# Optimization experiments

Measured on AMD Instinct MI355X. Metric: run time of the kernel, lower is better.

## Reference

```python
import jax, jax.numpy as jnp
import numpy as np

B = 16384   # batch
S = 6       # fixed number of ABR frequencies
H = 8       # num_heads
HD = 64     # head_dim
D = H * HD  # model width = head_dim * num_heads


def _pe(d):
    # FrequencyPositionalEncoding: pe[i, 0::2] = sin(f_i * div), pe[i, 1::2] = cos(f_i * div)
    freqs = np.array([6.0, 12.0, 18.0, 24.0, 30.0, 0.0], np.float32) / 30.0
    div = np.exp(np.arange(0, d, 2, dtype=np.float32) * (-np.log(10000.0) / d))
    pe = np.zeros((S, d), np.float32)
    pe[:, 0::2] = np.sin(freqs[:, None] * div)
    pe[:, 1::2] = np.cos(freqs[:, None] * div)
    return jnp.asarray(pe)


def _freq_bias():
    # adjacent-frequency bias 0.1, octave pairs (0,1),(1,3) overwritten to 0.05
    b = np.zeros((S, S), np.float32)
    for i in range(S - 1):
        b[i, i + 1] = 0.1
        b[i + 1, i] = 0.1
    for i, j in [(0, 1), (1, 3)]:
        b[i, j] = 0.05
        b[j, i] = 0.05
    return jnp.asarray(b)


def setup_inputs() -> dict:
    key = jax.random.key(0)
    ks = jax.random.split(key, 6)

    def w(k, shape, s=0.05):
        return jax.random.normal(k, shape, jnp.float32) * s

    return {
        "x": jax.random.normal(ks[0], (B, S), jnp.float32),
        "W_in": w(ks[1], (1, D)), "b_in": jnp.zeros((D,), jnp.float32),
        "Wq": w(ks[2], (D, D)), "bq": jnp.zeros((D,), jnp.float32),
        "Wk": w(ks[3], (D, D)), "bk": jnp.zeros((D,), jnp.float32),
        "Wv": w(ks[4], (D, D)), "bv": jnp.zeros((D,), jnp.float32),
        "Wo": w(ks[5], (D, 1)), "bo": jnp.zeros((1,), jnp.float32),
        "gamma": jnp.ones((D,), jnp.float32),
        "beta": jnp.zeros((D,), jnp.float32),
    }


def reference(x, W_in, b_in, Wq, bq, Wk, bk, Wv, bv, Wo, bo, gamma, beta):
    Bn, Sn = x.shape
    Dn = gamma.shape[0]
    hd = Dn // H
    # input projection: scalar token -> D   (Linear(1, D))
    tok = x[..., None] * W_in[0] + b_in                      # (B, S, D)
    tok = tok + _pe(Dn)[None]                                # frequency positional encoding
    # LayerNorm (eps=1e-5)
    mu = tok.mean(-1, keepdims=True)
    var = tok.var(-1, keepdims=True)
    tok = (tok - mu) * jax.lax.rsqrt(var + 1e-5) * gamma + beta
    # q/k/v projections, split heads
    q = (tok @ Wq + bq).reshape(Bn, Sn, H, hd)
    k = (tok @ Wk + bk).reshape(Bn, Sn, H, hd)
    v = (tok @ Wv + bv).reshape(Bn, Sn, H, hd)
    scores = jnp.einsum('bihd,bjhd->bhij', q, k) * (hd ** -0.5)
    scores = scores + _freq_bias()[None, None]               # (B, H, S, S)
    attn = jax.nn.softmax(scores, axis=-1)                   # dropout = identity (eval)
    attended = jnp.einsum('bhij,bjhd->bihd', attn, v).reshape(Bn, Sn, Dn)
    out = (attended @ Wo + bo)[..., 0] + x                   # (B, S) residual
    return out, attn.mean(axis=1)
```

## Files before the change

### kernel.cpp

```cpp
#include <hip/hip_runtime.h>
#include <math.h>

#define WS_STATS 0
#define WS_T     16
#define WS_LS    600

__constant__ float FREQ_BIAS[36] = {
    0.0f, 0.05f, 0.0f, 0.0f, 0.0f, 0.0f,
    0.05f, 0.0f, 0.1f, 0.05f, 0.0f, 0.0f,
    0.0f, 0.1f, 0.0f, 0.1f, 0.0f, 0.0f,
    0.0f, 0.05f, 0.1f, 0.0f, 0.1f, 0.0f,
    0.0f, 0.0f, 0.0f, 0.1f, 0.0f, 0.1f,
    0.0f, 0.0f, 0.0f, 0.0f, 0.1f, 0.0f
};

__global__ __launch_bounds__(512) void kP(const float* __restrict__ W_in,
                                          const float* __restrict__ b_in,
                                          const float* __restrict__ gamma,
                                          const float* __restrict__ beta,
                                          float* __restrict__ ws)
{
    __shared__ float red[13][8];
    const int d = threadIdx.x, wave = d >> 6, lane = d & 63;

    const float k_ln = 0.0179889457300305367f;
    const float freqs[6] = {0.2f, 0.4f, 0.6f, 0.8f, 1.0f, 0.0f};
    const float wd = W_in[d];
    const float gm = gamma[d];
    const float bt = beta[d];
    const float bi = b_in[d];
    const float dv = __expf(-(float)(d & ~1) * k_ln);
    const bool odd = (d & 1);
    float c[6];
    #pragma unroll
    for (int s = 0; s < 6; ++s) {
        float ph = freqs[s] * dv;
        c[s] = bi + (odd ? __cosf(ph) : __sinf(ph));
    }

    float sums[7];
    sums[0] = wd;
    #pragma unroll
    for (int s = 0; s < 6; ++s) sums[1 + s] = c[s];
    #pragma unroll
    for (int m = 1; m < 64; m <<= 1) {
        #pragma unroll
        for (int k = 0; k < 7; ++k) sums[k] += __shfl_xor(sums[k], m, 64);
    }
    if (lane == 0) {
        #pragma unroll
        for (int k = 0; k < 7; ++k) red[k][wave] = sums[k];
    }
    __syncthreads();
    float mw = 0.f, mc[6] = {0.f, 0.f, 0.f, 0.f, 0.f, 0.f};
    #pragma unroll
    for (int j = 0; j < 8; ++j) mw += red[0][j];
    mw *= (1.0f / 512.0f);
    #pragma unroll
    for (int s = 0; s < 6; ++s) {
        float t = 0.f;
        #pragma unroll
        for (int j = 0; j < 8; ++j) t += red[1 + s][j];
        mc[s] = t * (1.0f / 512.0f);
    }
    __syncthreads();

    const float hw = wd - mw;
    float hc[6];
    #pragma unroll
    for (int s = 0; s < 6; ++s) hc[s] = c[s] - mc[s];

    float moms[13];
    moms[0] = hw * hw;
    #pragma unroll
    for (int s = 0; s < 6; ++s) { moms[1 + s] = hw * hc[s]; moms[7 + s] = hc[s] * hc[s]; }
    #pragma unroll
    for (int m = 1; m < 64; m <<= 1) {
        #pragma unroll
        for (int k = 0; k < 13; ++k) moms[k] += __shfl_xor(moms[k], m, 64);
    }
    if (lane == 0) {
        #pragma unroll
        for (int k = 0; k < 13; ++k) red[k][wave] = moms[k];
    }
    __syncthreads();
    if (d < 13) {
        float t = 0.f;
        #pragma unroll
        for (int j = 0; j < 8; ++j) t += red[d][j];
        ws[WS_STATS + d] = t * (1.0f / 512.0f);
    }

    float4 f0 = make_float4(hw * gm, hc[0] * gm, hc[1] * gm, hc[2] * gm);
    float4 f1 = make_float4(hc[3] * gm, hc[4] * gm, hc[5] * gm, bt);
    *(float4*)&ws[WS_LS + d * 8]     = f0;
    *(float4*)&ws[WS_LS + d * 8 + 4] = f1;
}

__global__ __launch_bounds__(512) void kA(
    const float* __restrict__ Wq, const float* __restrict__ bq,
    const float* __restrict__ Wk, const float* __restrict__ bk,
    const float* __restrict__ Wv, const float* __restrict__ bv,
    const float* __restrict__ ws, float* __restrict__ part)
{
    __shared__ float ls_s[64 * 8];
    __shared__ float partial[8][8][64];

    const int tid = threadIdx.x, wave = tid >> 6, lane = tid & 63;
    const int bid = blockIdx.x;
    const int rc = bid & 7, cg = (bid >> 3) & 7, p = bid >> 6;

    ls_s[tid] = ws[WS_LS + rc * 512 + tid];
    __syncthreads();

    const float* W  = (p == 0) ? Wq : ((p == 1) ? Wk : Wv);
    const float* bb = (p == 0) ? bq : ((p == 1) ? bk : bv);
    const int col = (cg << 6) | lane;
    const int lr0 = wave << 3;
    const int row0 = (rc << 6) | lr0;

    float acc[8] = {0.f, 0.f, 0.f, 0.f, 0.f, 0.f, 0.f, 0.f};
    #pragma unroll
    for (int rr = 0; rr < 8; ++rr) {
        const float wv = W[(row0 + rr) * 512 + col];
        const float4 f0 = *(const float4*)&ls_s[(lr0 + rr) * 8];
        const float4 f1 = *(const float4*)&ls_s[(lr0 + rr) * 8 + 4];
        acc[0] = fmaf(wv, f0.x, acc[0]);
        acc[1] = fmaf(wv, f0.y, acc[1]);
        acc[2] = fmaf(wv, f0.z, acc[2]);
        acc[3] = fmaf(wv, f0.w, acc[3]);
        acc[4] = fmaf(wv, f1.x, acc[4]);
        acc[5] = fmaf(wv, f1.y, acc[5]);
        acc[6] = fmaf(wv, f1.z, acc[6]);
        acc[7] = fmaf(wv, f1.w, acc[7]);
    }
    #pragma unroll
    for (int v = 0; v < 8; ++v) partial[wave][v][lane] = acc[v];
    __syncthreads();

    {
        const int v = tid >> 6, cx = tid & 63;
        float t = 0.f;
        #pragma unroll
        for (int w = 0; w < 8; ++w) t += partial[w][v][cx];
        if (v == 7 && rc == 0) t += bb[(cg << 6) | cx];
        part[(size_t)bid * 512 + tid] = t;
    }
}

__global__ __launch_bounds__(256) void kB(const float* __restrict__ part,
                                          const float* __restrict__ Wo,
                                          float* __restrict__ ws)
{
    __shared__ float ab[24][65];
    const int tid = threadIdx.x;
    const int h = blockIdx.x;

    for (int e = tid; e < 24 * 64; e += 256) {
        const int vp = e >> 6, c = e & 63;
        const int p = vp >> 3, v = vp & 7;
        const int stripe = p * 8 + h;
        float t = 0.f;
        #pragma unroll
        for (int rcx = 0; rcx < 8; ++rcx)
            t += part[(size_t)(stripe * 8 + rcx) * 512 + v * 64 + c];
        ab[vp][c] = t;
    }
    __syncthreads();

    if (tid < 64) {
        const int a = tid >> 3, b2 = tid & 7;
        float acc = 0.f;
        #pragma unroll
        for (int c = 0; c < 64; ++c)
            acc = fmaf(ab[a][c], ab[8 + b2][c], acc);
        ws[WS_T + (h << 6) + tid] = acc * 0.125f;
    } else if (tid < 72) {
        const int a = tid - 64;
        float acc = 0.f;
        #pragma unroll
        for (int c = 0; c < 64; ++c)
            acc = fmaf(ab[16 + a][c], Wo[(h << 6) + c], acc);
        ws[WS_T + 512 + (h << 3) + a] = acc;
    }
}

__global__ __launch_bounds__(384) void kC(const float* __restrict__ x,
                                          const float* __restrict__ ws,
                                          const float* __restrict__ bo,
                                          float* __restrict__ out, int total)
{
    __shared__ float T_s[592];
    const int tid = threadIdx.x;
    for (int e = tid; e < 589; e += 384)
        T_s[e] = (e < 576) ? ws[WS_T + e] : ws[WS_STATS + (e - 576)];
    __syncthreads();

    const int g = blockIdx.x * 384 + tid;
    if (g >= total) return;
    const unsigned b = (unsigned)g / 6u;
    const int i = g - (int)b * 6;

    const float* D8 = T_s;
    const float* VD = T_s + 512;
    const float vw = T_s[576];
    const float* cov = T_s + 577;
    const float* vc = T_s + 583;
    const float bo0 = bo[0];

    const float2* xp = (const float2*)(x + (size_t)b * 6u);
    const float2 x01 = xp[0], x23 = xp[1], x45 = xp[2];
    const float al[6] = {x01.x, x01.y, x23.x, x23.y, x45.x, x45.y};

    float r[6], u[6];
    #pragma unroll
    for (int j = 0; j < 6; ++j) {
        float a = al[j];
        float var = fmaf(a, fmaf(a, vw, 2.0f * cov[j]), vc[j]) + 1e-5f;
        r[j] = rsqrtf(var);
        u[j] = a * r[j];
    }
    float bias[6];
    #pragma unroll
    for (int j = 0; j < 6; ++j) bias[j] = FREQ_BIAS[i * 6 + j];

    const float r_i = r[i], u_i = u[i];
    float acc = 0.f;
    float am[6] = {0.f, 0.f, 0.f, 0.f, 0.f, 0.f};

    #pragma unroll
    for (int h = 0; h < 8; ++h) {
        const float* Dh = D8 + h * 64;
        const float* Vh = VD + h * 8;
        const float P1 = Dh[0], P5 = Dh[7], P7 = Dh[56], P9 = Dh[63];
        const float P3i = Dh[(1 + i) * 8], P6i = Dh[(1 + i) * 8 + 7];

        float s[6];
        #pragma unroll
        for (int j = 0; j < 6; ++j) {
            float t1 = fmaf(u[j], P1, fmaf(r[j], Dh[1 + j], P5));
            float t2 = fmaf(u[j], P3i, fmaf(r[j], Dh[(1 + i) * 8 + 1 + j], P6i));
            float t3 = fmaf(u[j], P7, fmaf(r[j], Dh[57 + j], P9));
            s[j] = fmaf(u_i, t1, fmaf(r_i, t2, t3)) + bias[j];
        }
        float m = s[0];
        #pragma unroll
        for (int j = 1; j < 6; ++j) m = fmaxf(m, s[j]);
        float e[6], ssum = 0.f;
        #pragma unroll
        for (int j = 0; j < 6; ++j) { e[j] = __expf(s[j] - m); ssum += e[j]; }
        const float inv = 1.0f / ssum;

        const float av = Vh[0], cvv = Vh[7];
        float ha = 0.f;
        #pragma unroll
        for (int j = 0; j < 6; ++j) {
            float a = e[j] * inv;
            am[j] += a;
            float vp = fmaf(u[j], av, r[j] * Vh[1 + j]);
            ha = fmaf(a, vp, ha);
        }
        acc += ha + cvv;
    }

    out[g] = acc + bo0 + al[i];
    float2* amp = (float2*)(out + total + (size_t)g * 6u);
    amp[0] = make_float2(am[0] * 0.125f, am[1] * 0.125f);
    amp[1] = make_float2(am[2] * 0.125f, am[3] * 0.125f);
    amp[2] = make_float2(am[4] * 0.125f, am[5] * 0.125f);
}

extern "C" void kernel_launch(void* const* d_in, const int* in_sizes, int n_in,
                              void* d_out, int out_size, void* d_ws, size_t ws_size,
                              hipStream_t stream) {
    const float* x     = (const float*)d_in[0];
    const float* W_in  = (const float*)d_in[1];
    const float* b_in  = (const float*)d_in[2];
    const float* Wq    = (const float*)d_in[3];
    const float* bq    = (const float*)d_in[4];
    const float* Wk    = (const float*)d_in[5];
    const float* bk    = (const float*)d_in[6];
    const float* Wv    = (const float*)d_in[7];
    const float* bv    = (const float*)d_in[8];
    const float* Wo    = (const float*)d_in[9];
    const float* bo    = (const float*)d_in[10];
    const float* gamma = (const float*)d_in[11];
    const float* beta  = (const float*)d_in[12];
    float* ws  = (float*)d_ws;
    float* out = (float*)d_out;

    const int total = in_sizes[0];

    kP<<<1, 512, 0, stream>>>(W_in, b_in, gamma, beta, ws);
    kA<<<192, 512, 0, stream>>>(Wq, bq, Wk, bk, Wv, bv, ws, out);
    kB<<<8, 256, 0, stream>>>(out, Wo, ws);
    kC<<<256, 384, 0, stream>>>(x, ws, bo, out, total);
}
```

Baseline: 22.90 us.

## Fuse LayerNorm stats, QKV projection and head reduction into one kernel

Merges the three precompute kernels (LayerNorm moment stats, partial QKV projections, per-head reduction) into a single 8-block, 1024-thread kernel. Each block recomputes the LN stats redundantly and handles one head's columns across all 512 rows for Q, K and V. This removes two launches and the global round trip of the partial sums. In exchange only 8 blocks stream the 3 MB of weights, so memory-level parallelism is much lower. The final batch kernel block size also changes from 384 to 256.

Result: slower. 25.77 us (+12.5%).

```diff
diff --git a/kernel.cpp b/kernel.cpp
--- a/kernel.cpp
+++ b/kernel.cpp
@@ -3,7 +3,6 @@
 
 #define WS_STATS 0
 #define WS_T     16
-#define WS_LS    600
 
 __constant__ float FREQ_BIAS[36] = {
     0.0f, 0.05f, 0.0f, 0.0f, 0.0f, 0.0f,
@@ -14,189 +13,173 @@
     0.0f, 0.0f, 0.0f, 0.0f, 0.1f, 0.0f
 };
 
-__global__ __launch_bounds__(512) void kP(const float* __restrict__ W_in,
-                                          const float* __restrict__ b_in,
-                                          const float* __restrict__ gamma,
-                                          const float* __restrict__ beta,
-                                          float* __restrict__ ws)
-{
-    __shared__ float red[13][8];
-    const int d = threadIdx.x, wave = d >> 6, lane = d & 63;
-
-    const float k_ln = 0.0179889457300305367f;
-    const float freqs[6] = {0.2f, 0.4f, 0.6f, 0.8f, 1.0f, 0.0f};
-    const float wd = W_in[d];
-    const float gm = gamma[d];
-    const float bt = beta[d];
-    const float bi = b_in[d];
-    const float dv = __expf(-(float)(d & ~1) * k_ln);
-    const bool odd = (d & 1);
-    float c[6];
-    #pragma unroll
-    for (int s = 0; s < 6; ++s) {
-        float ph = freqs[s] * dv;
-        c[s] = bi + (odd ? __cosf(ph) : __sinf(ph));
-    }
-
-    float sums[7];
-    sums[0] = wd;
-    #pragma unroll
-    for (int s = 0; s < 6; ++s) sums[1 + s] = c[s];
-    #pragma unroll
-    for (int m = 1; m < 64; m <<= 1) {
-        #pragma unroll
-        for (int k = 0; k < 7; ++k) sums[k] += __shfl_xor(sums[k], m, 64);
-    }
-    if (lane == 0) {
-        #pragma unroll
-        for (int k = 0; k < 7; ++k) red[k][wave] = sums[k];
-    }
-    __syncthreads();
-    float mw = 0.f, mc[6] = {0.f, 0.f, 0.f, 0.f, 0.f, 0.f};
-    #pragma unroll
-    for (int j = 0; j < 8; ++j) mw += red[0][j];
-    mw *= (1.0f / 512.0f);
-    #pragma unroll
-    for (int s = 0; s < 6; ++s) {
-        float t = 0.f;
-        #pragma unroll
-        for (int j = 0; j < 8; ++j) t += red[1 + s][j];
-        mc[s] = t * (1.0f / 512.0f);
-    }
-    __syncthreads();
-
-    const float hw = wd - mw;
-    float hc[6];
-    #pragma unroll
-    for (int s = 0; s < 6; ++s) hc[s] = c[s] - mc[s];
-
-    float moms[13];
-    moms[0] = hw * hw;
-    #pragma unroll
-    for (int s = 0; s < 6; ++s) { moms[1 + s] = hw * hc[s]; moms[7 + s] = hc[s] * hc[s]; }
-    #pragma unroll
-    for (int m = 1; m < 64; m <<= 1) {
-        #pragma unroll
-        for (int k = 0; k < 13; ++k) moms[k] += __shfl_xor(moms[k], m, 64);
-    }
-    if (lane == 0) {
-        #pragma unroll
-        for (int k = 0; k < 13; ++k) red[k][wave] = moms[k];
-    }
-    __syncthreads();
-    if (d < 13) {
-        float t = 0.f;
-        #pragma unroll
-        for (int j = 0; j < 8; ++j) t += red[d][j];
-        ws[WS_STATS + d] = t * (1.0f / 512.0f);
-    }
-
-    float4 f0 = make_float4(hw * gm, hc[0] * gm, hc[1] * gm, hc[2] * gm);
-    float4 f1 = make_float4(hc[3] * gm, hc[4] * gm, hc[5] * gm, bt);
-    *(float4*)&ws[WS_LS + d * 8]     = f0;
-    *(float4*)&ws[WS_LS + d * 8 + 4] = f1;
-}
-
-__global__ __launch_bounds__(512) void kA(
+__global__ __launch_bounds__(1024) void kH(
+    const float* __restrict__ W_in, const float* __restrict__ b_in,
+    const float* __restrict__ gamma, const float* __restrict__ beta,
     const float* __restrict__ Wq, const float* __restrict__ bq,
     const float* __restrict__ Wk, const float* __restrict__ bk,
     const float* __restrict__ Wv, const float* __restrict__ bv,
-    const float* __restrict__ ws, float* __restrict__ part)
+    const float* __restrict__ Wo,
+    float* __restrict__ ws)
 {
-    __shared__ float ls_s[64 * 8];
-    __shared__ float partial[8][8][64];
+    __shared__ float ls8[512][8];
+    __shared__ float partial[16][8][64];
+    __shared__ float ab[24][65];
+    __shared__ float red[13][8];
 
     const int tid = threadIdx.x, wave = tid >> 6, lane = tid & 63;
-    const int bid = blockIdx.x;
-    const int rc = bid & 7, cg = (bid >> 3) & 7, p = bid >> 6;
-
-    ls_s[tid] = ws[WS_LS + rc * 512 + tid];
-    __syncthreads();
-
-    const float* W  = (p == 0) ? Wq : ((p == 1) ? Wk : Wv);
-    const float* bb = (p == 0) ? bq : ((p == 1) ? bk : bv);
-    const int col = (cg << 6) | lane;
-    const int lr0 = wave << 3;
-    const int row0 = (rc << 6) | lr0;
-
-    float acc[8] = {0.f, 0.f, 0.f, 0.f, 0.f, 0.f, 0.f, 0.f};
-    #pragma unroll
-    for (int rr = 0; rr < 8; ++rr) {
-        const float wv = W[(row0 + rr) * 512 + col];
-        const float4 f0 = *(const float4*)&ls_s[(lr0 + rr) * 8];
-        const float4 f1 = *(const float4*)&ls_s[(lr0 + rr) * 8 + 4];
-        acc[0] = fmaf(wv, f0.x, acc[0]);
-        acc[1] = fmaf(wv, f0.y, acc[1]);
-        acc[2] = fmaf(wv, f0.z, acc[2]);
-        acc[3] = fmaf(wv, f0.w, acc[3]);
-        acc[4] = fmaf(wv, f1.x, acc[4]);
-        acc[5] = fmaf(wv, f1.y, acc[5]);
-        acc[6] = fmaf(wv, f1.z, acc[6]);
-        acc[7] = fmaf(wv, f1.w, acc[7]);
-    }
-    #pragma unroll
-    for (int v = 0; v < 8; ++v) partial[wave][v][lane] = acc[v];
-    __syncthreads();
-
+    const int h = blockIdx.x;
+
+    float wd = 0.f, gm = 0.f, bt = 0.f, c[6];
+    if (tid < 512) {
+        const float k_ln = 0.0179889457300305367f;
+        const float freqs[6] = {0.2f, 0.4f, 0.6f, 0.8f, 1.0f, 0.0f};
+        wd = W_in[tid]; gm = gamma[tid]; bt = beta[tid];
+        const float bi = b_in[tid];
+        const float dv = __expf(-(float)(tid & ~1) * k_ln);
+        const bool odd = (tid & 1);
+        #pragma unroll
+        for (int s = 0; s < 6; ++s) {
+            float ph = freqs[s] * dv;
+            c[s] = bi + (odd ? __cosf(ph) : __sinf(ph));
+        }
+        float sums[7];
+        sums[0] = wd;
+        #pragma unroll
+        for (int s = 0; s < 6; ++s) sums[1 + s] = c[s];
+        #pragma unroll
+        for (int m = 1; m < 64; m <<= 1) {
+            #pragma unroll
+            for (int k = 0; k < 7; ++k) sums[k] += __shfl_xor(sums[k], m, 64);
+        }
+        if (lane == 0) {
+            #pragma unroll
+            for (int k = 0; k < 7; ++k) red[k][wave] = sums[k];
+        }
+    }
+    __syncthreads();
+    float mw = 0.f, mc[6];
     {
-        const int v = tid >> 6, cx = tid & 63;
-        float t = 0.f;
-        #pragma unroll
-        for (int w = 0; w < 8; ++w) t += partial[w][v][cx];
-        if (v == 7 && rc == 0) t += bb[(cg << 6) | cx];
-        part[(size_t)bid * 512 + tid] = t;
+        float t = 0.f;
+        #pragma unroll
+        for (int j = 0; j < 8; ++j) t += red[0][j];
+        mw = t * (1.0f / 512.0f);
+        #pragma unroll
+        for (int s = 0; s < 6; ++s) {
+            t = 0.f;
+            #pragma unroll
+            for (int j = 0; j < 8; ++j) t += red[1 + s][j];
+            mc[s] = t * (1.0f / 512.0f);
+        }
+    }
+    __syncthreads();
+    if (tid < 512) {
+        const float hw = wd - mw;
+        float hc[6];
+        #pragma unroll
+        for (int s = 0; s < 6; ++s) hc[s] = c[s] - mc[s];
+        float moms[13];
+        moms[0] = hw * hw;
+        #pragma unroll
+        for (int s = 0; s < 6; ++s) { moms[1 + s] = hw * hc[s]; moms[7 + s] = hc[s] * hc[s]; }
+        #pragma unroll
+        for (int m = 1; m < 64; m <<= 1) {
+            #pragma unroll
+            for (int k = 0; k < 13; ++k) moms[k] += __shfl_xor(moms[k], m, 64);
+        }
+        if (lane == 0) {
+            #pragma unroll
+            for (int k = 0; k < 13; ++k) red[k][wave] = moms[k];
+        }
+        ls8[tid][0] = hw * gm;
+        #pragma unroll
+        for (int s = 0; s < 6; ++s) ls8[tid][1 + s] = hc[s] * gm;
+        ls8[tid][7] = bt;
+    }
+    __syncthreads();
+    if (h == 0 && tid < 13) {
+        float t = 0.f;
+        #pragma unroll
+        for (int j = 0; j < 8; ++j) t += red[tid][j];
+        ws[WS_STATS + tid] = t * (1.0f / 512.0f);
+    }
+
+    const int colg = (h << 6) | lane;
+    const int row0 = wave << 5;
+    #pragma unroll
+    for (int p = 0; p < 3; ++p) {
+        const float* W  = (p == 0) ? Wq : ((p == 1) ? Wk : Wv);
+        const float* bb = (p == 0) ? bq : ((p == 1) ? bk : bv);
+
+        float acc[8] = {0.f, 0.f, 0.f, 0.f, 0.f, 0.f, 0.f, 0.f};
+        #pragma unroll 8
+        for (int rr = 0; rr < 32; ++rr) {
+            const int row = row0 + rr;
+            const float wv = W[row * 512 + colg];
+            const float4 f0 = *(const float4*)&ls8[row][0];
+            const float4 f1 = *(const float4*)&ls8[row][4];
+            acc[0] = fmaf(wv, f0.x, acc[0]);
+            acc[1] = fmaf(wv, f0.y, acc[1]);
+            acc[2] = fmaf(wv, f0.z, acc[2]);
+            acc[3] = fmaf(wv, f0.w, acc[3]);
+            acc[4] = fmaf(wv, f1.x, acc[4]);
+            acc[5] = fmaf(wv, f1.y, acc[5]);
+            acc[6] = fmaf(wv, f1.z, acc[6]);
+            acc[7] = fmaf(wv, f1.w, acc[7]);
+        }
+        #pragma unroll
+        for (int v = 0; v < 8; ++v) partial[wave][v][lane] = acc[v];
+        __syncthreads();
+        if (tid < 512) {
+            const int v = tid >> 6, cx = tid & 63;
+            float t = 0.f;
+            #pragma unroll
+            for (int w = 0; w < 16; ++w) t += partial[w][v][cx];
+            if (v == 7) t += bb[(h << 6) | cx];
+            ab[p * 8 + v][cx] = t;
+        }
+        __syncthreads();
+    }
+
+    if (tid < 512) {
+        const int entry = tid >> 3, seg = tid & 7;
+        const int a = entry >> 3, b2 = entry & 7;
+        const int c0 = seg << 3;
+        float t = 0.f;
+        #pragma unroll
+        for (int c = 0; c < 8; ++c)
+            t = fmaf(ab[a][c0 + c], ab[8 + b2][c0 + c], t);
+        t += __shfl_xor(t, 1, 64);
+        t += __shfl_xor(t, 2, 64);
+        t += __shfl_xor(t, 4, 64);
+        if (seg == 0) ws[WS_T + (h << 6) + entry] = t * 0.125f;
+    } else if (tid < 576) {
+        const int u = tid - 512;
+        const int a = u >> 3, seg = u & 7;
+        const int c0 = seg << 3;
+        float t = 0.f;
+        #pragma unroll
+        for (int c = 0; c < 8; ++c)
+            t = fmaf(ab[16 + a][c0 + c], Wo[(h << 6) + c0 + c], t);
+        t += __shfl_xor(t, 1, 64);
+        t += __shfl_xor(t, 2, 64);
+        t += __shfl_xor(t, 4, 64);
+        if (seg == 0) ws[WS_T + 512 + (h << 3) + a] = t;
     }
 }
 
-__global__ __launch_bounds__(256) void kB(const float* __restrict__ part,
-                                          const float* __restrict__ Wo,
-                                          float* __restrict__ ws)
-{
-    __shared__ float ab[24][65];
-    const int tid = threadIdx.x;
-    const int h = blockIdx.x;
-
-    for (int e = tid; e < 24 * 64; e += 256) {
-        const int vp = e >> 6, c = e & 63;
-        const int p = vp >> 3, v = vp & 7;
-        const int stripe = p * 8 + h;
-        float t = 0.f;
-        #pragma unroll
-        for (int rcx = 0; rcx < 8; ++rcx)
-            t += part[(size_t)(stripe * 8 + rcx) * 512 + v * 64 + c];
-        ab[vp][c] = t;
-    }
-    __syncthreads();
-
-    if (tid < 64) {
-        const int a = tid >> 3, b2 = tid & 7;
-        float acc = 0.f;
-        #pragma unroll
-        for (int c = 0; c < 64; ++c)
-            acc = fmaf(ab[a][c], ab[8 + b2][c], acc);
-        ws[WS_T + (h << 6) + tid] = acc * 0.125f;
-    } else if (tid < 72) {
-        const int a = tid - 64;
-        float acc = 0.f;
-        #pragma unroll
-        for (int c = 0; c < 64; ++c)
-            acc = fmaf(ab[16 + a][c], Wo[(h << 6) + c], acc);
-        ws[WS_T + 512 + (h << 3) + a] = acc;
-    }
-}
-
-__global__ __launch_bounds__(384) void kC(const float* __restrict__ x,
+__global__ __launch_bounds__(256) void kC(const float* __restrict__ x,
                                           const float* __restrict__ ws,
                                           const float* __restrict__ bo,
                                           float* __restrict__ out, int total)
 {
     __shared__ float T_s[592];
     const int tid = threadIdx.x;
-    for (int e = tid; e < 589; e += 384)
+    for (int e = tid; e < 589; e += 256)
         T_s[e] = (e < 576) ? ws[WS_T + e] : ws[WS_STATS + (e - 576)];
     __syncthreads();
 
-    const int g = blockIdx.x * 384 + tid;
+    const int g = blockIdx.x * 256 + tid;
     if (g >= total) return;
     const unsigned b = (unsigned)g / 6u;
     const int i = g - (int)b * 6;
@@ -291,8 +274,6 @@
 
     const int total = in_sizes[0];
 
-    kP<<<1, 512, 0, stream>>>(W_in, b_in, gamma, beta, ws);
-    kA<<<192, 512, 0, stream>>>(Wq, bq, Wk, bk, Wv, bv, ws, out);
-    kB<<<8, 256, 0, stream>>>(out, Wo, ws);
-    kC<<<256, 384, 0, stream>>>(x, ws, bo, out, total);
+    kH<<<8, 1024, 0, stream>>>(W_in, b_in, gamma, beta, Wq, bq, Wk, bk, Wv, bv, Wo, ws);
+    kC<<<(total + 255) / 256, 256, 0, stream>>>(x, ws, bo, out, total);
 }
```
